# Performance work log

Hardware: AMD Instinct MI355X
Metric: run time of the kernel (lower is better)

Reference implementation:

```python
import jax, jax.numpy as jnp
import numpy as np

N = 8192
IN_F = 512
OUT_F = 128
NEG_BIG = -9.0e15


def setup_inputs() -> dict:
    key = jax.random.key(0)
    k_x, k_adj, k_w, k_a1, k_a2 = jax.random.split(key, 5)
    X = jax.random.normal(k_x, (N, IN_F), dtype=jnp.float32)
    adj = jax.random.randint(k_adj, (N, N), 0, 2, dtype=jnp.int32)
    # xavier_uniform with gain=1.414
    gain = 1.414
    lim_w = gain * np.sqrt(6.0 / (IN_F + OUT_F))
    W = jax.random.uniform(k_w, (IN_F, OUT_F), minval=-lim_w, maxval=lim_w, dtype=jnp.float32)
    lim_a = gain * np.sqrt(6.0 / (OUT_F + 1))
    a_1 = jax.random.uniform(k_a1, (OUT_F, 1), minval=-lim_a, maxval=lim_a, dtype=jnp.float32)
    a_2 = jax.random.uniform(k_a2, (OUT_F, 1), minval=-lim_a, maxval=lim_a, dtype=jnp.float32)
    return {"X": X, "adj": adj, "W": W, "a_1": a_1, "a_2": a_2}


def reference(X, adj, W, a_1, a_2):
    h = X @ W                         # [N, out]
    Wh1 = h @ a_1                     # [N, 1]
    Wh2 = h @ a_2                     # [N, 1]
    alpha = Wh1 + Wh2.T               # [N, N] broadcast score sum
    s = jax.nn.sigmoid(alpha)
    masked = jnp.where(adj > 0, s, jnp.float32(NEG_BIG))
    attn = jax.nn.softmax(masked, axis=1)  # dropout p=0.0 -> identity
    return attn @ h                   # [N, out]
```

## Files before the change

kernel.cpp:

```cpp
#include <hip/hip_runtime.h>
#include <hip/hip_bf16.h>

#define N_NODES 8192
#define IN_F 512
#define OUT_F 128
#define KSHIFT 4
#define KP (1 << KSHIFT)
#define KT_PER (256 >> KSHIFT)
#define LOG2E 1.4426950408889634f

typedef unsigned short u16;
typedef unsigned int u32;
typedef short s16x8 __attribute__((ext_vector_type(8)));
typedef float f32x4 __attribute__((ext_vector_type(4)));
typedef u32 u32x4 __attribute__((ext_vector_type(4)));

__device__ __forceinline__ u16 f2bf(float f) {
    union { float f; unsigned u; } x; x.f = f;
    unsigned r = x.u + 0x7FFFu + ((x.u >> 16) & 1u);
    return (u16)(r >> 16);
}

__device__ __forceinline__ u32 packbf2(float a, float b) {
    __hip_bfloat162 h = __float22bfloat162_rn(make_float2(a, b));
    u32 u; __builtin_memcpy(&u, &h, 4);
    return u;
}

__device__ __forceinline__ float edge_p(float wh1, float w2, int keep) {
    float alpha = wh1 + w2;
    float e = exp2f(-LOG2E * alpha);
    float s = __builtin_amdgcn_rcpf(1.0f + e);
    float p = exp2f(LOG2E * s);
    return keep ? p : 0.0f;
}

__global__ void repack_W(const float* __restrict__ W, u16* __restrict__ W_frag) {
    int tid = blockIdx.x * 256 + threadIdx.x;
    int j = tid & 7;
    int lane = (tid >> 3) & 63;
    int nt = (tid >> 9) & 7;
    int kt = tid >> 12;
    int k = kt * 32 + (lane >> 4) * 8 + j;
    int n = nt * 16 + (lane & 15);
    W_frag[tid] = f2bf(W[k * OUT_F + n]);
}

__global__ void compute_Wa(const float* __restrict__ W, const float* __restrict__ a1,
                           const float* __restrict__ a2,
                           float* __restrict__ Wa1, float* __restrict__ Wa2) {
    int k = blockIdx.x * 256 + threadIdx.x;
    if (k >= IN_F) return;
    float s1 = 0.f, s2 = 0.f;
    #pragma unroll 8
    for (int n = 0; n < OUT_F; n++) {
        float w = W[k * OUT_F + n];
        s1 += w * a1[n];
        s2 += w * a2[n];
    }
    Wa1[k] = s1; Wa2[k] = s2;
}

__global__ __launch_bounds__(256)
void gemm_h(const float* __restrict__ X, const u16* __restrict__ W_frag,
            const float* __restrict__ Wa1, const float* __restrict__ Wa2,
            float* __restrict__ Wh1, float* __restrict__ Wh2,
            u16* __restrict__ h_frag) {
    int tid = threadIdx.x;
    int wave = tid >> 6;
    int lane = tid & 63;
    int quad = lane >> 4;
    int lid = lane & 15;
    int rbase = blockIdx.x * 16;
    const float* xrow = X + (size_t)(rbase + lid) * IN_F;
    const s16x8* Wf = (const s16x8*)W_frag;
    f32x4 acc0 = {}, acc1 = {};
    float p1 = 0.f, p2 = 0.f;
    int nt0 = wave * 2;

    for (int kt = 0; kt < 16; kt++) {
        int k0 = kt * 32 + quad * 8;
        float4 x0 = *(const float4*)(xrow + k0);
        float4 x1 = *(const float4*)(xrow + k0 + 4);
        u32x4 uv;
        uv.x = packbf2(x0.x, x0.y); uv.y = packbf2(x0.z, x0.w);
        uv.z = packbf2(x1.x, x1.y); uv.w = packbf2(x1.z, x1.w);
        s16x8 a = __builtin_bit_cast(s16x8, uv);
        if (wave == 0) {
            float4 wa = *(const float4*)(Wa1 + k0);
            float4 wb = *(const float4*)(Wa1 + k0 + 4);
            float4 wc = *(const float4*)(Wa2 + k0);
            float4 wd = *(const float4*)(Wa2 + k0 + 4);
            p1 += x0.x*wa.x + x0.y*wa.y + x0.z*wa.z + x0.w*wa.w
                + x1.x*wb.x + x1.y*wb.y + x1.z*wb.z + x1.w*wb.w;
            p2 += x0.x*wc.x + x0.y*wc.y + x0.z*wc.z + x0.w*wc.w
                + x1.x*wd.x + x1.y*wd.y + x1.z*wd.z + x1.w*wd.w;
        }
        s16x8 b0 = Wf[(kt * 8 + nt0) * 64 + lane];
        s16x8 b1 = Wf[(kt * 8 + nt0 + 1) * 64 + lane];
        acc0 = __builtin_amdgcn_mfma_f32_16x16x32_bf16(a, b0, acc0, 0, 0, 0);
        acc1 = __builtin_amdgcn_mfma_f32_16x16x32_bf16(a, b1, acc1, 0, 0, 0);
    }

    #pragma unroll
    for (int reg = 0; reg < 4; reg++) {
        int row = rbase + quad * 4 + reg;
        int ktile = row >> 5, kl = row & 31;
        int lane2 = (kl >> 3) * 16 + lid, j2 = kl & 7;
        h_frag[(size_t)((ktile * 8 + nt0) * 64 + lane2) * 8 + j2] = f2bf(acc0[reg]);
        h_frag[(size_t)((ktile * 8 + nt0 + 1) * 64 + lane2) * 8 + j2] = f2bf(acc1[reg]);
    }
    if (wave == 0) {
        p1 += __shfl_xor(p1, 16, 64); p1 += __shfl_xor(p1, 32, 64);
        p2 += __shfl_xor(p2, 16, 64); p2 += __shfl_xor(p2, 32, 64);
        if (lane < 16) { Wh1[rbase + lid] = p1; Wh2[rbase + lid] = p2; }
    }
}

__global__ __launch_bounds__(256)
void attn_kernel(const int* __restrict__ adj, const float* __restrict__ Wh1,
                 const float* __restrict__ Wh2, const u16* __restrict__ h_frag,
                 float* __restrict__ out_part, float* __restrict__ sum_part) {
    int tid = threadIdx.x;
    int wave = tid >> 6;
    int lane = tid & 63;
    int quad = lane >> 4;
    int lid = lane & 15;
    int rtile = blockIdx.x >> KSHIFT;
    int kh = blockIdx.x & (KP - 1);
    int rbase = rtile * 128 + wave * 32;
    int r0 = rbase + lid, r1 = r0 + 16;

    float wh10 = Wh1[r0], wh11 = Wh1[r1];
    f32x4 acc0[8] = {}, acc1[8] = {};
    float ps0 = 0.f, ps1 = 0.f;
    const s16x8* Hf = (const s16x8*)h_frag;
    const int* adjrow0 = adj + (size_t)r0 * N_NODES;
    const int* adjrow1 = adj + (size_t)r1 * N_NODES;

    const int kt0 = kh * KT_PER;
    const int ktend = kt0 + KT_PER;

    int kpf = kt0 * 32 + quad * 8;
    int4 A0a = *(const int4*)(adjrow0 + kpf);
    int4 A0b = *(const int4*)(adjrow0 + kpf + 4);
    int4 A1a = *(const int4*)(adjrow1 + kpf);
    int4 A1b = *(const int4*)(adjrow1 + kpf + 4);

    #pragma unroll 1
    for (int kt = kt0; kt < ktend; kt++) {
        int k0 = kt * 32 + quad * 8;
        int4 aj0a = A0a, aj0b = A0b, aj1a = A1a, aj1b = A1b;
        int ktn = (kt + 1 < ktend) ? (kt + 1) : kt;
        int k0n = ktn * 32 + quad * 8;
        A0a = *(const int4*)(adjrow0 + k0n);
        A0b = *(const int4*)(adjrow0 + k0n + 4);
        A1a = *(const int4*)(adjrow1 + k0n);
        A1b = *(const int4*)(adjrow1 + k0n + 4);

        float4 w20 = *(const float4*)(Wh2 + k0);
        float4 w21 = *(const float4*)(Wh2 + k0 + 4);

        float e0 = edge_p(wh10, w20.x, aj0a.x), e1 = edge_p(wh10, w20.y, aj0a.y);
        float e2 = edge_p(wh10, w20.z, aj0a.z), e3 = edge_p(wh10, w20.w, aj0a.w);
        float e4 = edge_p(wh10, w21.x, aj0b.x), e5 = edge_p(wh10, w21.y, aj0b.y);
        float e6 = edge_p(wh10, w21.z, aj0b.z), e7 = edge_p(wh10, w21.w, aj0b.w);
        ps0 += ((e0 + e1) + (e2 + e3)) + ((e4 + e5) + (e6 + e7));
        u32x4 uv0;
        uv0.x = packbf2(e0, e1); uv0.y = packbf2(e2, e3);
        uv0.z = packbf2(e4, e5); uv0.w = packbf2(e6, e7);

        float f0 = edge_p(wh11, w20.x, aj1a.x), f1 = edge_p(wh11, w20.y, aj1a.y);
        float f2 = edge_p(wh11, w20.z, aj1a.z), f3 = edge_p(wh11, w20.w, aj1a.w);
        float f4 = edge_p(wh11, w21.x, aj1b.x), f5 = edge_p(wh11, w21.y, aj1b.y);
        float f6 = edge_p(wh11, w21.z, aj1b.z), f7 = edge_p(wh11, w21.w, aj1b.w);
        ps1 += ((f0 + f1) + (f2 + f3)) + ((f4 + f5) + (f6 + f7));
        u32x4 uv1;
        uv1.x = packbf2(f0, f1); uv1.y = packbf2(f2, f3);
        uv1.z = packbf2(f4, f5); uv1.w = packbf2(f6, f7);

        s16x8 af0 = __builtin_bit_cast(s16x8, uv0);
        s16x8 af1 = __builtin_bit_cast(s16x8, uv1);

        #pragma unroll
        for (int nt = 0; nt < 8; nt++) {
            s16x8 b = Hf[(kt * 8 + nt) * 64 + lane];
            acc0[nt] = __builtin_amdgcn_mfma_f32_16x16x32_bf16(af0, b, acc0[nt], 0, 0, 0);
            acc1[nt] = __builtin_amdgcn_mfma_f32_16x16x32_bf16(af1, b, acc1[nt], 0, 0, 0);
        }
    }

    ps0 += __shfl_xor(ps0, 16, 64); ps0 += __shfl_xor(ps0, 32, 64);
    ps1 += __shfl_xor(ps1, 16, 64); ps1 += __shfl_xor(ps1, 32, 64);
    if (quad == 0) {
        sum_part[(size_t)kh * N_NODES + r0] = ps0;
        sum_part[(size_t)kh * N_NODES + r1] = ps1;
    }

    #pragma unroll
    for (int nt = 0; nt < 8; nt++) {
        #pragma unroll
        for (int reg = 0; reg < 4; reg++) {
            int row0 = rbase + quad * 4 + reg;
            int col = nt * 16 + lid;
            out_part[((size_t)kh * N_NODES + row0) * OUT_F + col] = acc0[nt][reg];
            out_part[((size_t)kh * N_NODES + row0 + 16) * OUT_F + col] = acc1[nt][reg];
        }
    }
}

__global__ void finalize(const float* __restrict__ out_part,
                         const float* __restrict__ sum_part,
                         float* __restrict__ out) {
    int gid = blockIdx.x * 256 + threadIdx.x;
    int i = gid >> 7;
    float s = 0.f, v = 0.f;
    for (int kh = 0; kh < KP; kh++) {
        s += sum_part[(size_t)kh * N_NODES + i];
        v += out_part[(size_t)kh * N_NODES * OUT_F + gid];
    }
    out[gid] = v / s;
}

extern "C" void kernel_launch(void* const* d_in, const int* in_sizes, int n_in,
                              void* d_out, int out_size, void* d_ws, size_t ws_size,
                              hipStream_t stream) {
    const float* X   = (const float*)d_in[0];
    const int*   adj = (const int*)d_in[1];
    const float* W   = (const float*)d_in[2];
    const float* a1  = (const float*)d_in[3];
    const float* a2  = (const float*)d_in[4];

    const size_t BASE = (size_t)4 << 20;
    char* ws = (char*)d_ws;
    float* Wh1 = (float*)(ws);
    float* Wh2 = (float*)(ws + (32 << 10));
    float* Wa1 = (float*)(ws + (64 << 10));
    float* Wa2 = (float*)(ws + (66 << 10));
    u16* W_frag = (u16*)(ws + (128 << 10));
    u16* h_frag = (u16*)(ws + (256 << 10));
    float* out_part = (float*)(ws + BASE);
    float* sum_part = (float*)(ws + BASE + ((size_t)KP << 22));
    float* out = (float*)d_out;

    hipLaunchKernelGGL(repack_W, dim3(256), dim3(256), 0, stream, W, W_frag);
    hipLaunchKernelGGL(compute_Wa, dim3(2), dim3(256), 0, stream, W, a1, a2, Wa1, Wa2);
    hipLaunchKernelGGL(gemm_h, dim3(512), dim3(256), 0, stream,
                       X, W_frag, Wa1, Wa2, Wh1, Wh2, h_frag);
    hipLaunchKernelGGL(attn_kernel, dim3(64 * KP), dim3(256), 0, stream,
                       adj, Wh1, Wh2, h_frag, out_part, sum_part);
    hipLaunchKernelGGL(finalize, dim3((N_NODES * OUT_F) / 256), dim3(256), 0, stream,
                       out_part, sum_part, out);
}
```

Measured before the change: 422.6 us.

## Fuse attention and finalize with full-row blocks sharing P tiles via LDS

```diff
diff --git a/kernel.cpp b/kernel.cpp
--- a/kernel.cpp
+++ b/kernel.cpp
@@ -4,9 +4,7 @@
 #define N_NODES 8192
 #define IN_F 512
 #define OUT_F 128
-#define KSHIFT 4
-#define KP (1 << KSHIFT)
-#define KT_PER (256 >> KSHIFT)
+#define NCHUNK (N_NODES / 256)
 #define LOG2E 1.4426950408889634f
 
 typedef unsigned short u16;
@@ -117,109 +115,103 @@
     }
 }
 
-__global__ __launch_bounds__(256)
-void attn_kernel(const int* __restrict__ adj, const float* __restrict__ Wh1,
-                 const float* __restrict__ Wh2, const u16* __restrict__ h_frag,
-                 float* __restrict__ out_part, float* __restrict__ sum_part) {
+__global__ __launch_bounds__(512)
+void attn_fused(const int* __restrict__ adj, const float* __restrict__ Wh1,
+                const float* __restrict__ Wh2, const u16* __restrict__ h_frag,
+                float* __restrict__ out) {
+    __shared__ u32x4 Plds[2][8][2][64];
+    __shared__ float rsum_lds[8][32];
+
     int tid = threadIdx.x;
     int wave = tid >> 6;
     int lane = tid & 63;
     int quad = lane >> 4;
     int lid = lane & 15;
-    int rtile = blockIdx.x >> KSHIFT;
-    int kh = blockIdx.x & (KP - 1);
-    int rbase = rtile * 128 + wave * 32;
+    int rbase = blockIdx.x * 32;
     int r0 = rbase + lid, r1 = r0 + 16;
 
     float wh10 = Wh1[r0], wh11 = Wh1[r1];
-    f32x4 acc0[8] = {}, acc1[8] = {};
+    f32x4 acc_lo = {}, acc_hi = {};
     float ps0 = 0.f, ps1 = 0.f;
     const s16x8* Hf = (const s16x8*)h_frag;
     const int* adjrow0 = adj + (size_t)r0 * N_NODES;
     const int* adjrow1 = adj + (size_t)r1 * N_NODES;
 
-    const int kt0 = kh * KT_PER;
-    const int ktend = kt0 + KT_PER;
-
-    int kpf = kt0 * 32 + quad * 8;
-    int4 A0a = *(const int4*)(adjrow0 + kpf);
-    int4 A0b = *(const int4*)(adjrow0 + kpf + 4);
-    int4 A1a = *(const int4*)(adjrow1 + kpf);
-    int4 A1b = *(const int4*)(adjrow1 + kpf + 4);
-
-    #pragma unroll 1
-    for (int kt = kt0; kt < ktend; kt++) {
-        int k0 = kt * 32 + quad * 8;
-        int4 aj0a = A0a, aj0b = A0b, aj1a = A1a, aj1b = A1b;
-        int ktn = (kt + 1 < ktend) ? (kt + 1) : kt;
-        int k0n = ktn * 32 + quad * 8;
+    int k0p = wave * 32 + quad * 8;
+    int4 A0a = *(const int4*)(adjrow0 + k0p);
+    int4 A0b = *(const int4*)(adjrow0 + k0p + 4);
+    int4 A1a = *(const int4*)(adjrow1 + k0p);
+    int4 A1b = *(const int4*)(adjrow1 + k0p + 4);
+    float4 W2a = *(const float4*)(Wh2 + k0p);
+    float4 W2b = *(const float4*)(Wh2 + k0p + 4);
+
+    #pragma unroll 2
+    for (int c = 0; c < NCHUNK; c++) {
+        float e0 = edge_p(wh10, W2a.x, A0a.x), e1 = edge_p(wh10, W2a.y, A0a.y);
+        float e2 = edge_p(wh10, W2a.z, A0a.z), e3 = edge_p(wh10, W2a.w, A0a.w);
+        float e4 = edge_p(wh10, W2b.x, A0b.x), e5 = edge_p(wh10, W2b.y, A0b.y);
+        float e6 = edge_p(wh10, W2b.z, A0b.z), e7 = edge_p(wh10, W2b.w, A0b.w);
+        ps0 += ((e0 + e1) + (e2 + e3)) + ((e4 + e5) + (e6 + e7));
+        u32x4 uv0;
+        uv0.x = packbf2(e0, e1); uv0.y = packbf2(e2, e3);
+        uv0.z = packbf2(e4, e5); uv0.w = packbf2(e6, e7);
+
+        float f0 = edge_p(wh11, W2a.x, A1a.x), f1 = edge_p(wh11, W2a.y, A1a.y);
+        float f2 = edge_p(wh11, W2a.z, A1a.z), f3 = edge_p(wh11, W2a.w, A1a.w);
+        float f4 = edge_p(wh11, W2b.x, A1b.x), f5 = edge_p(wh11, W2b.y, A1b.y);
+        float f6 = edge_p(wh11, W2b.z, A1b.z), f7 = edge_p(wh11, W2b.w, A1b.w);
+        ps1 += ((f0 + f1) + (f2 + f3)) + ((f4 + f5) + (f6 + f7));
+        u32x4 uv1;
+        uv1.x = packbf2(f0, f1); uv1.y = packbf2(f2, f3);
+        uv1.z = packbf2(f4, f5); uv1.w = packbf2(f6, f7);
+
+        Plds[c & 1][wave][0][lane] = uv0;
+        Plds[c & 1][wave][1][lane] = uv1;
+
+        int cn = (c + 1 < NCHUNK) ? c + 1 : c;
+        int k0n = (cn * 8 + wave) * 32 + quad * 8;
         A0a = *(const int4*)(adjrow0 + k0n);
         A0b = *(const int4*)(adjrow0 + k0n + 4);
         A1a = *(const int4*)(adjrow1 + k0n);
         A1b = *(const int4*)(adjrow1 + k0n + 4);
-
-        float4 w20 = *(const float4*)(Wh2 + k0);
-        float4 w21 = *(const float4*)(Wh2 + k0 + 4);
-
-        float e0 = edge_p(wh10, w20.x, aj0a.x), e1 = edge_p(wh10, w20.y, aj0a.y);
-        float e2 = edge_p(wh10, w20.z, aj0a.z), e3 = edge_p(wh10, w20.w, aj0a.w);
-        float e4 = edge_p(wh10, w21.x, aj0b.x), e5 = edge_p(wh10, w21.y, aj0b.y);
-        float e6 = edge_p(wh10, w21.z, aj0b.z), e7 = edge_p(wh10, w21.w, aj0b.w);
-        ps0 += ((e0 + e1) + (e2 + e3)) + ((e4 + e5) + (e6 + e7));
-        u32x4 uv0;
-        uv0.x = packbf2(e0, e1); uv0.y = packbf2(e2, e3);
-        uv0.z = packbf2(e4, e5); uv0.w = packbf2(e6, e7);
-
-        float f0 = edge_p(wh11, w20.x, aj1a.x), f1 = edge_p(wh11, w20.y, aj1a.y);
-        float f2 = edge_p(wh11, w20.z, aj1a.z), f3 = edge_p(wh11, w20.w, aj1a.w);
-        float f4 = edge_p(wh11, w21.x, aj1b.x), f5 = edge_p(wh11, w21.y, aj1b.y);
-        float f6 = edge_p(wh11, w21.z, aj1b.z), f7 = edge_p(wh11, w21.w, aj1b.w);
-        ps1 += ((f0 + f1) + (f2 + f3)) + ((f4 + f5) + (f6 + f7));
-        u32x4 uv1;
-        uv1.x = packbf2(f0, f1); uv1.y = packbf2(f2, f3);
-        uv1.z = packbf2(f4, f5); uv1.w = packbf2(f6, f7);
-
-        s16x8 af0 = __builtin_bit_cast(s16x8, uv0);
-        s16x8 af1 = __builtin_bit_cast(s16x8, uv1);
+        W2a = *(const float4*)(Wh2 + k0n);
+        W2b = *(const float4*)(Wh2 + k0n + 4);
+
+        asm volatile("s_waitcnt lgkmcnt(0)" ::: "memory");
+        __builtin_amdgcn_s_barrier();
+        asm volatile("" ::: "memory");
+        __builtin_amdgcn_sched_barrier(0);
 
         #pragma unroll
-        for (int nt = 0; nt < 8; nt++) {
-            s16x8 b = Hf[(kt * 8 + nt) * 64 + lane];
-            acc0[nt] = __builtin_amdgcn_mfma_f32_16x16x32_bf16(af0, b, acc0[nt], 0, 0, 0);
-            acc1[nt] = __builtin_amdgcn_mfma_f32_16x16x32_bf16(af1, b, acc1[nt], 0, 0, 0);
+        for (int j = 0; j < 8; j++) {
+            s16x8 af0 = __builtin_bit_cast(s16x8, Plds[c & 1][j][0][lane]);
+            s16x8 af1 = __builtin_bit_cast(s16x8, Plds[c & 1][j][1][lane]);
+            s16x8 b = Hf[((c * 8 + j) * 8 + wave) * 64 + lane];
+            acc_lo = __builtin_amdgcn_mfma_f32_16x16x32_bf16(af0, b, acc_lo, 0, 0, 0);
+            acc_hi = __builtin_amdgcn_mfma_f32_16x16x32_bf16(af1, b, acc_hi, 0, 0, 0);
         }
     }
 
     ps0 += __shfl_xor(ps0, 16, 64); ps0 += __shfl_xor(ps0, 32, 64);
     ps1 += __shfl_xor(ps1, 16, 64); ps1 += __shfl_xor(ps1, 32, 64);
-    if (quad == 0) {
-        sum_part[(size_t)kh * N_NODES + r0] = ps0;
-        sum_part[(size_t)kh * N_NODES + r1] = ps1;
-    }
+    if (lane < 16) {
+        rsum_lds[wave][lane] = ps0;
+        rsum_lds[wave][lane + 16] = ps1;
+    }
+    __syncthreads();
 
     #pragma unroll
-    for (int nt = 0; nt < 8; nt++) {
+    for (int reg = 0; reg < 4; reg++) {
+        int row = quad * 4 + reg;
+        float slo = 0.f, shi = 0.f;
         #pragma unroll
-        for (int reg = 0; reg < 4; reg++) {
-            int row0 = rbase + quad * 4 + reg;
-            int col = nt * 16 + lid;
-            out_part[((size_t)kh * N_NODES + row0) * OUT_F + col] = acc0[nt][reg];
-            out_part[((size_t)kh * N_NODES + row0 + 16) * OUT_F + col] = acc1[nt][reg];
+        for (int w = 0; w < 8; w++) {
+            slo += rsum_lds[w][row];
+            shi += rsum_lds[w][row + 16];
         }
-    }
-}
-
-__global__ void finalize(const float* __restrict__ out_part,
-                         const float* __restrict__ sum_part,
-                         float* __restrict__ out) {
-    int gid = blockIdx.x * 256 + threadIdx.x;
-    int i = gid >> 7;
-    float s = 0.f, v = 0.f;
-    for (int kh = 0; kh < KP; kh++) {
-        s += sum_part[(size_t)kh * N_NODES + i];
-        v += out_part[(size_t)kh * N_NODES * OUT_F + gid];
-    }
-    out[gid] = v / s;
+        out[(size_t)(rbase + row) * OUT_F + wave * 16 + lid] = acc_lo[reg] / slo;
+        out[(size_t)(rbase + row + 16) * OUT_F + wave * 16 + lid] = acc_hi[reg] / shi;
+    }
 }
 
 extern "C" void kernel_launch(void* const* d_in, const int* in_sizes, int n_in,
@@ -231,7 +223,6 @@
     const float* a1  = (const float*)d_in[3];
     const float* a2  = (const float*)d_in[4];
 
-    const size_t BASE = (size_t)4 << 20;
     char* ws = (char*)d_ws;
     float* Wh1 = (float*)(ws);
     float* Wh2 = (float*)(ws + (32 << 10));
@@ -239,16 +230,12 @@
     float* Wa2 = (float*)(ws + (66 << 10));
     u16* W_frag = (u16*)(ws + (128 << 10));
     u16* h_frag = (u16*)(ws + (256 << 10));
-    float* out_part = (float*)(ws + BASE);
-    float* sum_part = (float*)(ws + BASE + ((size_t)KP << 22));
     float* out = (float*)d_out;
 
     hipLaunchKernelGGL(repack_W, dim3(256), dim3(256), 0, stream, W, W_frag);
     hipLaunchKernelGGL(compute_Wa, dim3(2), dim3(256), 0, stream, W, a1, a2, Wa1, Wa2);
     hipLaunchKernelGGL(gemm_h, dim3(512), dim3(256), 0, stream,
                        X, W_frag, Wa1, Wa2, Wh1, Wh2, h_frag);
-    hipLaunchKernelGGL(attn_kernel, dim3(64 * KP), dim3(256), 0, stream,
-                       adj, Wh1, Wh2, h_frag, out_part, sum_part);
-    hipLaunchKernelGGL(finalize, dim3((N_NODES * OUT_F) / 256), dim3(256), 0, stream,
-                       out_part, sum_part, out);
-}
+    hipLaunchKernelGGL(attn_fused, dim3(N_NODES / 32), dim3(512), 0, stream,
+                       adj, Wh1, Wh2, h_frag, out);
+}
```

Measured after the change: 536.6 us. +27.0%, slower.

## Fuse split-K attention partials into one block with LDS reduction

Applied to the files above, without the earlier changes.

```diff
diff --git a/kernel.cpp b/kernel.cpp
--- a/kernel.cpp
+++ b/kernel.cpp
@@ -4,9 +4,8 @@
 #define N_NODES 8192
 #define IN_F 512
 #define OUT_F 128
-#define KSHIFT 4
-#define KP (1 << KSHIFT)
-#define KT_PER (256 >> KSHIFT)
+#define NWAVE 16
+#define KT_PER (256 / NWAVE)
 #define LOG2E 1.4426950408889634f
 
 typedef unsigned short u16;
@@ -117,18 +116,19 @@
     }
 }
 
-__global__ __launch_bounds__(256)
-void attn_kernel(const int* __restrict__ adj, const float* __restrict__ Wh1,
-                 const float* __restrict__ Wh2, const u16* __restrict__ h_frag,
-                 float* __restrict__ out_part, float* __restrict__ sum_part) {
+__global__ __launch_bounds__(1024, 4)
+void attn_fused(const int* __restrict__ adj, const float* __restrict__ Wh1,
+                const float* __restrict__ Wh2, const u16* __restrict__ h_frag,
+                float* __restrict__ out) {
+    __shared__ f32x4 red[8][16][64];
+    __shared__ float rsum_lds[NWAVE][32];
+
     int tid = threadIdx.x;
     int wave = tid >> 6;
     int lane = tid & 63;
     int quad = lane >> 4;
     int lid = lane & 15;
-    int rtile = blockIdx.x >> KSHIFT;
-    int kh = blockIdx.x & (KP - 1);
-    int rbase = rtile * 128 + wave * 32;
+    int rbase = blockIdx.x * 32;
     int r0 = rbase + lid, r1 = r0 + 16;
 
     float wh10 = Wh1[r0], wh11 = Wh1[r1];
@@ -138,7 +138,7 @@
     const int* adjrow0 = adj + (size_t)r0 * N_NODES;
     const int* adjrow1 = adj + (size_t)r1 * N_NODES;
 
-    const int kt0 = kh * KT_PER;
+    const int kt0 = wave * KT_PER;
     const int ktend = kt0 + KT_PER;
 
     int kpf = kt0 * 32 + quad * 8;
@@ -192,34 +192,52 @@
 
     ps0 += __shfl_xor(ps0, 16, 64); ps0 += __shfl_xor(ps0, 32, 64);
     ps1 += __shfl_xor(ps1, 16, 64); ps1 += __shfl_xor(ps1, 32, 64);
-    if (quad == 0) {
-        sum_part[(size_t)kh * N_NODES + r0] = ps0;
-        sum_part[(size_t)kh * N_NODES + r1] = ps1;
+    if (lane < 16) {
+        rsum_lds[wave][lane] = ps0;
+        rsum_lds[wave][lane + 16] = ps1;
     }
 
     #pragma unroll
-    for (int nt = 0; nt < 8; nt++) {
+    for (int s = 8; s >= 1; s >>= 1) {
+        if (wave >= s && wave < 2 * s) {
+            #pragma unroll
+            for (int nt = 0; nt < 8; nt++) {
+                red[wave - s][nt][lane] = acc0[nt];
+                red[wave - s][nt + 8][lane] = acc1[nt];
+            }
+        }
+        __syncthreads();
+        if (wave < s) {
+            #pragma unroll
+            for (int nt = 0; nt < 8; nt++) {
+                acc0[nt] += red[wave][nt][lane];
+                acc1[nt] += red[wave][nt + 8][lane];
+            }
+        }
+        __syncthreads();
+    }
+
+    if (wave == 0) {
         #pragma unroll
         for (int reg = 0; reg < 4; reg++) {
-            int row0 = rbase + quad * 4 + reg;
-            int col = nt * 16 + lid;
-            out_part[((size_t)kh * N_NODES + row0) * OUT_F + col] = acc0[nt][reg];
-            out_part[((size_t)kh * N_NODES + row0 + 16) * OUT_F + col] = acc1[nt][reg];
-        }
-    }
-}
-
-__global__ void finalize(const float* __restrict__ out_part,
-                         const float* __restrict__ sum_part,
-                         float* __restrict__ out) {
-    int gid = blockIdx.x * 256 + threadIdx.x;
-    int i = gid >> 7;
-    float s = 0.f, v = 0.f;
-    for (int kh = 0; kh < KP; kh++) {
-        s += sum_part[(size_t)kh * N_NODES + i];
-        v += out_part[(size_t)kh * N_NODES * OUT_F + gid];
-    }
-    out[gid] = v / s;
+            int row = quad * 4 + reg;
+            float slo = 0.f, shi = 0.f;
+            #pragma unroll
+            for (int w = 0; w < NWAVE; w++) {
+                slo += rsum_lds[w][row];
+                shi += rsum_lds[w][row + 16];
+            }
+            float rlo = __builtin_amdgcn_rcpf(slo);
+            float rhi = __builtin_amdgcn_rcpf(shi);
+            rlo = rlo * (2.0f - slo * rlo);
+            rhi = rhi * (2.0f - shi * rhi);
+            #pragma unroll
+            for (int nt = 0; nt < 8; nt++) {
+                out[(size_t)(rbase + row) * OUT_F + nt * 16 + lid] = acc0[nt][reg] * rlo;
+                out[(size_t)(rbase + row + 16) * OUT_F + nt * 16 + lid] = acc1[nt][reg] * rhi;
+            }
+        }
+    }
 }
 
 extern "C" void kernel_launch(void* const* d_in, const int* in_sizes, int n_in,
@@ -231,7 +249,6 @@
     const float* a1  = (const float*)d_in[3];
     const float* a2  = (const float*)d_in[4];
 
-    const size_t BASE = (size_t)4 << 20;
     char* ws = (char*)d_ws;
     float* Wh1 = (float*)(ws);
     float* Wh2 = (float*)(ws + (32 << 10));
@@ -239,16 +256,12 @@
     float* Wa2 = (float*)(ws + (66 << 10));
     u16* W_frag = (u16*)(ws + (128 << 10));
     u16* h_frag = (u16*)(ws + (256 << 10));
-    float* out_part = (float*)(ws + BASE);
-    float* sum_part = (float*)(ws + BASE + ((size_t)KP << 22));
     float* out = (float*)d_out;
 
     hipLaunchKernelGGL(repack_W, dim3(256), dim3(256), 0, stream, W, W_frag);
     hipLaunchKernelGGL(compute_Wa, dim3(2), dim3(256), 0, stream, W, a1, a2, Wa1, Wa2);
     hipLaunchKernelGGL(gemm_h, dim3(512), dim3(256), 0, stream,
                        X, W_frag, Wa1, Wa2, Wh1, Wh2, h_frag);
-    hipLaunchKernelGGL(attn_kernel, dim3(64 * KP), dim3(256), 0, stream,
-                       adj, Wh1, Wh2, h_frag, out_part, sum_part);
-    hipLaunchKernelGGL(finalize, dim3((N_NODES * OUT_F) / 256), dim3(256), 0, stream,
-                       out_part, sum_part, out);
-}
+    hipLaunchKernelGGL(attn_fused, dim3(N_NODES / 32), dim3(1024), 0, stream,
+                       adj, Wh1, Wh2, h_frag, out);
+}
```

New measurement: 459.6 us. 8.7% more time.
